# Performance work log

Hardware: AMD Instinct MI355X
Metric: run time of the kernel (lower is better)

Reference implementation:

```python
import jax, jax.numpy as jnp
import numpy as np

TEMPERATURE = 0.07
EPS = 1e-9


def setup_inputs() -> dict:
    key = jax.random.key(0)
    k1, k2, k3 = jax.random.split(key, 3)
    N, D = 8192, 64
    return {
        "query_embeddings": jax.random.normal(k1, (N, D), dtype=jnp.float32),
        "key_embeddings": jax.random.normal(k2, (N, D), dtype=jnp.float32),
        "positive_indices": jax.random.randint(k3, (N,), 0, N),
    }


def _uhg_distances(q, k):
    # Projective (Minkowski signature +...+ -) hyperbolic distance, vectorized cdist-style.
    # inner(a,b) = sum(a_spatial * b_spatial) - a_time * b_time  (last coord is timelike)
    inner_qk = jnp.einsum('nd,md->nm', q[:, :-1], k[:, :-1]) - jnp.outer(q[:, -1], k[:, -1])
    inner_qq = jnp.sum(q[:, :-1] * q[:, :-1], axis=-1) - q[:, -1] * q[:, -1]  # [N]
    inner_kk = jnp.sum(k[:, :-1] * k[:, :-1], axis=-1) - k[:, -1] * k[:, -1]  # [M]
    denom = jnp.sqrt(jnp.maximum(jnp.abs(inner_qq[:, None] * inner_kk[None, :]), EPS))
    ratio = jnp.maximum(jnp.abs(inner_qk) / denom, 1.0 + EPS)
    return jnp.arccosh(ratio)  # [N, M]


def reference(query_embeddings, key_embeddings, positive_indices):
    N = query_embeddings.shape[0]
    distances = _uhg_distances(query_embeddings, key_embeddings)      # [N, N]
    similarities = -distances / TEMPERATURE                           # [N, N]
    # Faithful vectorization of the per-row loop:
    #   logits_i = sims[i] - sims[i, pos_i];  loss_i = -logits_i[0] + logsumexp(logits_i)
    pos_sim = jnp.take_along_axis(similarities, positive_indices[:, None], axis=1)  # [N,1]
    logits = similarities - pos_sim                                   # [N, N]
    per_row = -logits[:, 0] + jax.scipy.special.logsumexp(logits, axis=1)
    infonce_loss = jnp.sum(per_row) / N
    return infonce_loss, similarities, distances
```

## Files before the change

### kernel.cpp

```cpp
#include <hip/hip_runtime.h>
#include <hip/hip_bf16.h>
#include <math.h>


#define NN 8192
#define DD 64

static constexpr float EPSV      = 1e-9f;
static constexpr float NEG_INV_T = -1.0f / 0.07f;

typedef const __attribute__((address_space(1))) unsigned int* gas_u32p;
typedef __attribute__((address_space(3))) unsigned int* las_u32p;

__device__ __forceinline__ void load_lds16(const void* g, void* l) {
    __builtin_amdgcn_global_load_lds((gas_u32p)g, (las_u32p)l, 16, 0, 0);
}

__global__ __launch_bounds__(256) void uhg_transpose_negate(
    const float* __restrict__ K, float* __restrict__ Kt)
{
    __shared__ float T[64][65];
    const int tid = threadIdx.x;
    const int j0  = blockIdx.x * 64;
    {
        const int j = tid >> 2;
        const int c = (tid & 3) * 16;
        const float* src = K + (size_t)(j0 + j) * DD + c;
        #pragma unroll
        for (int u = 0; u < 4; ++u) {
            const float4 v = *reinterpret_cast<const float4*>(src + 4 * u);
            T[j][c + 4*u + 0] = v.x;
            T[j][c + 4*u + 1] = v.y;
            T[j][c + 4*u + 2] = v.z;
            T[j][c + 4*u + 3] = v.w;
        }
    }
    __syncthreads();
    {
        const int d = tid >> 2;
        const int c = (tid & 3) * 16;
        const float sgn = (d == 63) ? -1.0f : 1.0f;
        float* dst = Kt + (size_t)d * NN + j0 + c;
        #pragma unroll
        for (int u = 0; u < 4; ++u) {
            float4 v;
            v.x = sgn * T[c + 4*u + 0][d];
            v.y = sgn * T[c + 4*u + 1][d];
            v.z = sgn * T[c + 4*u + 2][d];
            v.w = sgn * T[c + 4*u + 3][d];
            *reinterpret_cast<float4*>(dst + 4 * u) = v;
        }
    }
}

__global__ __launch_bounds__(256) void uhg_qqkk(
    const float* __restrict__ Q, const float* __restrict__ K,
    float* __restrict__ qq, float* __restrict__ kk)
{
    const int i = blockIdx.x * 256 + threadIdx.x;
    const bool isQ = (i < NN);
    const int r = isQ ? i : (i - NN);
    const float* src = (isQ ? Q : K) + (size_t)r * DD;
    float acc = 0.0f;
    #pragma unroll
    for (int c = 0; c < 15; ++c) {
        const float4 v = *reinterpret_cast<const float4*>(src + 4 * c);
        acc += v.x*v.x + v.y*v.y + v.z*v.z + v.w*v.w;
    }
    const float4 v = *reinterpret_cast<const float4*>(src + 60);
    acc += v.x*v.x + v.y*v.y + v.z*v.z;
    acc -= v.w*v.w;
    (isQ ? qq : kk)[r] = acc;
}

__global__ __launch_bounds__(256) void uhg_main(
    const float* __restrict__ Q, const float* __restrict__ Kt,
    const float* __restrict__ qq, const float* __restrict__ kk,
    float* __restrict__ out_sims, float* __restrict__ out_dist,
    float* __restrict__ Spart, float* __restrict__ sim0part)
{
    constexpr int TM = 32, TN = 256, NT = 4096 / TN;

    __shared__ float Qs[DD][36];
    __shared__ float Ks[DD][260];

    const int tid  = threadIdx.x;
    const int tx   = tid & 63;
    const int ty   = tid >> 6;
    const int half = blockIdx.x & 1;
    const int row0 = (blockIdx.x >> 1) * TM;
    const int chalf = half * 4096;
    const int wrow = 8 * ty;

    {
        const int r  = tid >> 3;
        const int dc = (tid & 7) * 8;
        const float* src = Q + (size_t)(row0 + r) * DD + dc;
        const float4 v0 = *reinterpret_cast<const float4*>(src);
        const float4 v1 = *reinterpret_cast<const float4*>(src + 4);
        Qs[dc + 0][r] = v0.x;  Qs[dc + 1][r] = v0.y;
        Qs[dc + 2][r] = v0.z;  Qs[dc + 3][r] = v0.w;
        Qs[dc + 4][r] = v1.x;  Qs[dc + 5][r] = v1.y;
        Qs[dc + 6][r] = v1.z;  Qs[dc + 7][r] = v1.w;
    }

    float rq[8];
    {
        const float4 a = *reinterpret_cast<const float4*>(qq + row0 + wrow);
        const float4 b = *reinterpret_cast<const float4*>(qq + row0 + wrow + 4);
        rq[0]=a.x; rq[1]=a.y; rq[2]=a.z; rq[3]=a.w;
        rq[4]=b.x; rq[5]=b.y; rq[6]=b.z; rq[7]=b.w;
    }

    float s[8]     = {0,0,0,0,0,0,0,0};
    float sim0r[8] = {0,0,0,0,0,0,0,0};

    float* ps[8];
    float* pd[8];
    #pragma unroll
    for (int rr = 0; rr < 8; ++rr) {
        const size_t rowoff = (size_t)(row0 + wrow + rr) * NN + chalf + tx;
        ps[rr] = out_sims + rowoff;
        pd[rr] = out_dist + rowoff;
    }

    for (int t = 0; t < NT; ++t) {
        const int c0 = t * TN;
        __syncthreads();

        {
            const int dbase = ty * 16;
            #pragma unroll
            for (int j = 0; j < 16; ++j) {
                const int d = dbase + j;
                load_lds16(Kt + (size_t)d * NN + chalf + c0 + 4 * tx, &Ks[d][0]);
            }
        }
        __syncthreads();

        float acc[8][4] = {};
        #pragma unroll 4
        for (int d = 0; d < DD; ++d) {
            const float4 qv0 = *reinterpret_cast<const float4*>(&Qs[d][wrow]);
            const float4 qv1 = *reinterpret_cast<const float4*>(&Qs[d][wrow + 4]);
            const float qa[8] = {qv0.x, qv0.y, qv0.z, qv0.w,
                                 qv1.x, qv1.y, qv1.z, qv1.w};
            float kv[4];
            kv[0] = Ks[d][tx];
            kv[1] = Ks[d][tx + 64];
            kv[2] = Ks[d][tx + 128];
            kv[3] = Ks[d][tx + 192];
            #pragma unroll
            for (int rr = 0; rr < 8; ++rr)
                #pragma unroll
                for (int i = 0; i < 4; ++i)
                    acc[rr][i] = fmaf(qa[rr], kv[i], acc[rr][i]);
        }

        float rk[4];
        rk[0] = kk[chalf + c0 + tx];
        rk[1] = kk[chalf + c0 + tx + 64];
        rk[2] = kk[chalf + c0 + tx + 128];
        rk[3] = kk[chalf + c0 + tx + 192];

        #pragma unroll
        for (int rr = 0; rr < 8; ++rr) {
            #pragma unroll
            for (int i = 0; i < 4; ++i) {
                const float inner = acc[rr][i];
                const float dd = fmaxf(fabsf(rq[rr] * rk[i]), EPSV);
                float dist = 0.0f, sim = 0.0f, e = 1.0f;
                if (inner * inner > dd * 0.9999f) {
                    const float ratio = fmaxf(fabsf(inner) / sqrtf(dd), 1.0f);
                    dist = __logf(ratio + sqrtf(fmaf(ratio, ratio, -1.0f)));
                    sim  = dist * NEG_INV_T;
                    e    = __expf(sim);
                }
                __builtin_nontemporal_store(dist, pd[rr] + c0 + 64 * i);
                __builtin_nontemporal_store(sim,  ps[rr] + c0 + 64 * i);
                if (half == 0 && t == 0 && i == 0 && tx == 0) sim0r[rr] = sim;
                s[rr] += e;
            }
        }
    }

    #pragma unroll
    for (int rr = 0; rr < 8; ++rr) {
        float v = s[rr];
        #pragma unroll
        for (int mask = 32; mask > 0; mask >>= 1)
            v += __shfl_xor(v, mask, 64);
        s[rr] = v;
    }
    if (tx == 0) {
        #pragma unroll
        for (int rr = 0; rr < 8; ++rr) {
            const int row = row0 + wrow + rr;
            Spart[half * NN + row] = s[rr];
            if (half == 0) sim0part[row] = sim0r[rr];
        }
    }
}

__global__ __launch_bounds__(256) void uhg_finalize(
    const float* __restrict__ Spart, const float* __restrict__ sim0part,
    float* __restrict__ out)
{
    __shared__ float red[256];
    const int tid = threadIdx.x;
    float a = 0.0f;
    for (int r = tid; r < NN; r += 256) {
        const float S = Spart[r] + Spart[NN + r];
        a += -sim0part[r] + logf(S);
    }
    red[tid] = a;
    __syncthreads();
    for (int off = 128; off > 0; off >>= 1) {
        if (tid < off) red[tid] += red[tid + off];
        __syncthreads();
    }
    if (tid == 0) out[0] = red[0] / (float)NN;
}

extern "C" void kernel_launch(void* const* d_in, const int* in_sizes, int n_in,
                              void* d_out, int out_size, void* d_ws, size_t ws_size,
                              hipStream_t stream)
{
    const float* Q = (const float*)d_in[0];
    const float* K = (const float*)d_in[1];

    float* out      = (float*)d_out;
    float* out_sims = out + 1;
    float* out_dist = out + 1 + (size_t)NN * NN;

    float* w        = (float*)d_ws;
    float* Kt       = w;
    float* qq       = w + 524288;
    float* kk       = w + 532480;
    float* Spart    = w + 540672;
    float* sim0part = w + 557056;

    uhg_transpose_negate<<<NN / 64, 256, 0, stream>>>(K, Kt);
    uhg_qqkk<<<2 * NN / 256, 256, 0, stream>>>(Q, K, qq, kk);
    uhg_main<<<512, 256, 0, stream>>>(Q, Kt, qq, kk, out_sims, out_dist,
                                      Spart, sim0part);
    uhg_finalize<<<1, 256, 0, stream>>>(Spart, sim0part, out);
}
```

Baseline: 743.8 us.

## Split columns into eight chunks and read K directly from global memory

The main kernel now gives each block one of eight 1024-column chunks instead of one of two halves, which launches 2048 blocks instead of 512 so more work is spread across the compute units. The LDS staging of K tiles and its two barriers per tile are removed, and K values are loaded straight from global memory, relying on the caches for reuse across the four warps. The finalize step sums eight partial row sums and the workspace layout is extended to hold them. The risk is more global/L2 traffic for K and fewer reuse opportunities than the shared-memory tile gave.

```diff
diff --git a/kernel.cpp b/kernel.cpp
--- a/kernel.cpp
+++ b/kernel.cpp
@@ -8,13 +8,6 @@
 
 static constexpr float EPSV      = 1e-9f;
 static constexpr float NEG_INV_T = -1.0f / 0.07f;
-
-typedef const __attribute__((address_space(1))) unsigned int* gas_u32p;
-typedef __attribute__((address_space(3))) unsigned int* las_u32p;
-
-__device__ __forceinline__ void load_lds16(const void* g, void* l) {
-    __builtin_amdgcn_global_load_lds((gas_u32p)g, (las_u32p)l, 16, 0, 0);
-}
 
 __global__ __launch_bounds__(256) void uhg_transpose_negate(
     const float* __restrict__ K, float* __restrict__ Kt)
@@ -79,18 +72,19 @@
     float* __restrict__ out_sims, float* __restrict__ out_dist,
     float* __restrict__ Spart, float* __restrict__ sim0part)
 {
-    constexpr int TM = 32, TN = 256, NT = 4096 / TN;
+    constexpr int TM = 32;
+    constexpr int CB = 1024;
+    constexpr int TN = 256;
 
     __shared__ float Qs[DD][36];
-    __shared__ float Ks[DD][260];
-
-    const int tid  = threadIdx.x;
-    const int tx   = tid & 63;
-    const int ty   = tid >> 6;
-    const int half = blockIdx.x & 1;
-    const int row0 = (blockIdx.x >> 1) * TM;
-    const int chalf = half * 4096;
-    const int wrow = 8 * ty;
+
+    const int tid   = threadIdx.x;
+    const int tx    = tid & 63;
+    const int ty    = tid >> 6;
+    const int cs    = blockIdx.x & 7;
+    const int row0  = (blockIdx.x >> 3) * TM;
+    const int cbase = cs * CB;
+    const int wrow  = 8 * ty;
 
     {
         const int r  = tid >> 3;
@@ -115,41 +109,25 @@
     float s[8]     = {0,0,0,0,0,0,0,0};
     float sim0r[8] = {0,0,0,0,0,0,0,0};
 
-    float* ps[8];
-    float* pd[8];
-    #pragma unroll
-    for (int rr = 0; rr < 8; ++rr) {
-        const size_t rowoff = (size_t)(row0 + wrow + rr) * NN + chalf + tx;
-        ps[rr] = out_sims + rowoff;
-        pd[rr] = out_dist + rowoff;
-    }
-
-    for (int t = 0; t < NT; ++t) {
-        const int c0 = t * TN;
-        __syncthreads();
-
-        {
-            const int dbase = ty * 16;
-            #pragma unroll
-            for (int j = 0; j < 16; ++j) {
-                const int d = dbase + j;
-                load_lds16(Kt + (size_t)d * NN + chalf + c0 + 4 * tx, &Ks[d][0]);
-            }
-        }
-        __syncthreads();
-
+    __syncthreads();
+
+    for (int t = 0; t < CB / TN; ++t) {
+        const int c0 = cbase + t * TN;
+        const float* kp = Kt + c0 + tx;
         float acc[8][4] = {};
-        #pragma unroll 4
+
+        #pragma unroll 8
         for (int d = 0; d < DD; ++d) {
             const float4 qv0 = *reinterpret_cast<const float4*>(&Qs[d][wrow]);
             const float4 qv1 = *reinterpret_cast<const float4*>(&Qs[d][wrow + 4]);
             const float qa[8] = {qv0.x, qv0.y, qv0.z, qv0.w,
                                  qv1.x, qv1.y, qv1.z, qv1.w};
+            const size_t off = (size_t)d * NN;
             float kv[4];
-            kv[0] = Ks[d][tx];
-            kv[1] = Ks[d][tx + 64];
-            kv[2] = Ks[d][tx + 128];
-            kv[3] = Ks[d][tx + 192];
+            kv[0] = kp[off];
+            kv[1] = kp[off + 64];
+            kv[2] = kp[off + 128];
+            kv[3] = kp[off + 192];
             #pragma unroll
             for (int rr = 0; rr < 8; ++rr)
                 #pragma unroll
@@ -158,27 +136,30 @@
         }
 
         float rk[4];
-        rk[0] = kk[chalf + c0 + tx];
-        rk[1] = kk[chalf + c0 + tx + 64];
-        rk[2] = kk[chalf + c0 + tx + 128];
-        rk[3] = kk[chalf + c0 + tx + 192];
+        rk[0] = kk[c0 + tx];
+        rk[1] = kk[c0 + tx + 64];
+        rk[2] = kk[c0 + tx + 128];
+        rk[3] = kk[c0 + tx + 192];
 
         #pragma unroll
         for (int rr = 0; rr < 8; ++rr) {
+            const size_t rowoff = (size_t)(row0 + wrow + rr) * NN + c0 + tx;
+            float* psr = out_sims + rowoff;
+            float* pdr = out_dist + rowoff;
             #pragma unroll
             for (int i = 0; i < 4; ++i) {
                 const float inner = acc[rr][i];
-                const float dd = fmaxf(fabsf(rq[rr] * rk[i]), EPSV);
+                const float dd2 = fmaxf(fabsf(rq[rr] * rk[i]), EPSV);
                 float dist = 0.0f, sim = 0.0f, e = 1.0f;
-                if (inner * inner > dd * 0.9999f) {
-                    const float ratio = fmaxf(fabsf(inner) / sqrtf(dd), 1.0f);
+                if (inner * inner > dd2 * 0.9999f) {
+                    const float ratio = fmaxf(fabsf(inner) / sqrtf(dd2), 1.0f);
                     dist = __logf(ratio + sqrtf(fmaf(ratio, ratio, -1.0f)));
                     sim  = dist * NEG_INV_T;
                     e    = __expf(sim);
                 }
-                __builtin_nontemporal_store(dist, pd[rr] + c0 + 64 * i);
-                __builtin_nontemporal_store(sim,  ps[rr] + c0 + 64 * i);
-                if (half == 0 && t == 0 && i == 0 && tx == 0) sim0r[rr] = sim;
+                __builtin_nontemporal_store(dist, pdr + 64 * i);
+                __builtin_nontemporal_store(sim,  psr + 64 * i);
+                if (cs == 0 && t == 0 && i == 0 && tx == 0) sim0r[rr] = sim;
                 s[rr] += e;
             }
         }
@@ -196,8 +177,8 @@
         #pragma unroll
         for (int rr = 0; rr < 8; ++rr) {
             const int row = row0 + wrow + rr;
-            Spart[half * NN + row] = s[rr];
-            if (half == 0) sim0part[row] = sim0r[rr];
+            Spart[cs * NN + row] = s[rr];
+            if (cs == 0) sim0part[row] = sim0r[rr];
         }
     }
 }
@@ -210,7 +191,9 @@
     const int tid = threadIdx.x;
     float a = 0.0f;
     for (int r = tid; r < NN; r += 256) {
-        const float S = Spart[r] + Spart[NN + r];
+        float S = 0.0f;
+        #pragma unroll
+        for (int q = 0; q < 8; ++q) S += Spart[q * NN + r];
         a += -sim0part[r] + logf(S);
     }
     red[tid] = a;
@@ -238,11 +221,11 @@
     float* qq       = w + 524288;
     float* kk       = w + 532480;
     float* Spart    = w + 540672;
-    float* sim0part = w + 557056;
+    float* sim0part = w + 606208;
 
     uhg_transpose_negate<<<NN / 64, 256, 0, stream>>>(K, Kt);
     uhg_qqkk<<<2 * NN / 256, 256, 0, stream>>>(Q, K, qq, kk);
-    uhg_main<<<512, 256, 0, stream>>>(Q, Kt, qq, kk, out_sims, out_dist,
-                                      Spart, sim0part);
+    uhg_main<<<2048, 256, 0, stream>>>(Q, Kt, qq, kk, out_sims, out_dist,
+                                       Spart, sim0part);
     uhg_finalize<<<1, 256, 0, stream>>>(Spart, sim0part, out);
 }
```

New measurement: 700.7 us. 5.8% less time.
